# Kernel optimization log

Hardware: AMD Instinct MI355X
Metric: run time of the kernel (lower is better)

## Reference

```python
import jax, jax.numpy as jnp
import numpy as np

R, T, XD, ZD = 4096, 2048, 8, 8
G_INIT = 4.595


def setup_inputs() -> dict:
    key = jax.random.key(0)
    k1, k2, k3, k4, k5 = jax.random.split(key, 5)
    X_t = jax.random.normal(k1, (T, XD), dtype=jnp.float32)
    Z_t = jax.random.normal(k2, (T, ZD), dtype=jnp.float32)
    G = jnp.full((R,), G_INIT, dtype=jnp.float32)
    eta = jnp.abs(jax.random.normal(k3, (R, XD), dtype=jnp.float32))
    zeta = jax.random.normal(k4, (R, ZD), dtype=jnp.float32)
    gamma = jax.random.normal(k5, (R, ZD), dtype=jnp.float32)
    return {"X_t": X_t, "Z_t": Z_t, "G": G, "eta": eta, "zeta": zeta, "gamma": gamma}


def _forward(X_t, Z_t, G, eta, zeta, gamma):
    # addSigmoid=True (training path): G_hat = sigmoid(G)
    G_hat = jax.nn.sigmoid(G)                       # [R]
    x_term = jnp.einsum('tx,rx->rt', X_t, eta)      # [R,T]  X_t . eta per run
    z_term = jnp.einsum('tz,rz->rt', Z_t, zeta)     # [R,T]  Z_t . zeta per run
    b = jnp.einsum('tz,rz->rt', Z_t, gamma)         # [R,T]  Z_t . gamma per run
    # theta_t = G_hat * theta_{t-1} + b_{t-1}, theta_0 = 0
    c = jnp.concatenate([jnp.zeros((b.shape[0], 1), b.dtype), b[:, :-1]], axis=1)
    a = jnp.broadcast_to(G_hat[:, None], c.shape)
    def combine(e1, e2):
        a1, u1 = e1
        a2, u2 = e2
        return (a1 * a2, a2 * u1 + u2)
    _, theta = jax.lax.associative_scan(combine, (a, c), axis=1)  # [R,T]
    return theta + x_term + z_term


def reference(X_t, Z_t, G, eta, zeta, gamma):
    return _forward(X_t, Z_t, G, eta, zeta, gamma)
```

## Files before the change

### kernel.cpp

```cpp
#include <hip/hip_runtime.h>
#include <math.h>

typedef float  f32x4  __attribute__((ext_vector_type(4)));
typedef short  bf16x8 __attribute__((ext_vector_type(8)));

namespace {
constexpr int R_RUNS  = 4096;
constexpr int T_STEPS = 2048;
constexpr int NKS     = 3;
constexpr size_t PA_ELEMS = (size_t)(R_RUNS / 16) * NKS * 4 * 16 * 8;
}

__device__ __forceinline__ float sigmoidf_(float x) { return 1.0f / (1.0f + expf(-x)); }

__device__ __forceinline__ unsigned short f2bf(float f) {
    unsigned u = __float_as_uint(f);
    unsigned r = (u + 0x7FFFu + ((u >> 16) & 1u)) >> 16;
    return (unsigned short)r;
}
__device__ __forceinline__ float bf2f(unsigned short h) {
    return __uint_as_float(((unsigned)h) << 16);
}
__device__ __forceinline__ float powg(float gh, int e) {
    float w = 1.f, p = gh;
    #pragma unroll
    for (int i = 0; i < 6; ++i) { w *= ((e >> i) & 1) ? p : 1.f; p *= p; }
    return w;
}

extern "C" __global__ __launch_bounds__(256)
void dlm_k1_pack(const float* __restrict__ Xt, const float* __restrict__ Zt,
                 const float* __restrict__ G, const float* __restrict__ eta,
                 const float* __restrict__ zeta, const float* __restrict__ gamma,
                 unsigned short* __restrict__ Pa, unsigned short* __restrict__ Qb)
{
    const int tid  = threadIdx.x;
    const int wid  = tid >> 6;
    const int lane = tid & 63;

    if (blockIdx.x >= 8) {
        const int pw = (blockIdx.x - 8) * 4 + wid;
        const int r  = pw * 64 + lane;
        const float4 e0 = *reinterpret_cast<const float4*>(eta   + (size_t)r * 8);
        const float4 e1 = *reinterpret_cast<const float4*>(eta   + (size_t)r * 8 + 4);
        const float4 c0 = *reinterpret_cast<const float4*>(zeta  + (size_t)r * 8);
        const float4 c1 = *reinterpret_cast<const float4*>(zeta  + (size_t)r * 8 + 4);
        const float4 m0 = *reinterpret_cast<const float4*>(gamma + (size_t)r * 8);
        const float4 m1 = *reinterpret_cast<const float4*>(gamma + (size_t)r * 8 + 4);
        const float pr[24] = {e0.x, e0.y, e0.z, e0.w, e1.x, e1.y, e1.z, e1.w,
                              c0.x, c0.y, c0.z, c0.w, c1.x, c1.y, c1.z, c1.w,
                              m0.x, m0.y, m0.z, m0.w, m1.x, m1.y, m1.z, m1.w};
        const int rt = r >> 4, rw = r & 15;
        #pragma unroll
        for (int s = 0; s < NKS; ++s) {
            #pragma unroll
            for (int ko = 0; ko < 4; ++ko) {
                union { unsigned short u[8]; uint4 v; } pk;
                #pragma unroll
                for (int i = 0; i < 8; ++i) {
                    const int k = s * 32 + ko * 8 + i;
                    unsigned short o;
                    if (k < 24)      o = f2bf(pr[k]);
                    else if (k < 48) o = f2bf(pr[k - 24]);
                    else if (k < 72) { const unsigned short h = f2bf(pr[k - 48]);
                                       o = f2bf(pr[k - 48] - bf2f(h)); }
                    else             o = 0;
                    pk.u[i] = o;
                }
                *reinterpret_cast<uint4*>(Pa + ((size_t)((rt * NKS + s) * 4 + ko) * 16 + rw) * 8) = pk.v;
            }
        }
        return;
    }

    const int wv = blockIdx.x * 4 + wid;
    const int t  = wv * 64 + lane;

    const float gh = sigmoidf_(G[0]);
    float gh64 = gh;
    #pragma unroll
    for (int i = 0; i < 6; ++i) gh64 *= gh64;

    const float4 za = *reinterpret_cast<const float4*>(Zt + (size_t)t * 8);
    const float4 zb = *reinterpret_cast<const float4*>(Zt + (size_t)t * 8 + 4);
    const float4 xa = *reinterpret_cast<const float4*>(Xt + (size_t)t * 8);
    const float4 xb = *reinterpret_cast<const float4*>(Xt + (size_t)t * 8 + 4);

    float acc[8] = {0.f, 0.f, 0.f, 0.f, 0.f, 0.f, 0.f, 0.f};
    for (int m = 0; m < wv; ++m) {
        const float* __restrict__ zp = Zt + (size_t)(m * 64 + lane) * 8;
        const float4 pa = *reinterpret_cast<const float4*>(zp);
        const float4 pb = *reinterpret_cast<const float4*>(zp + 4);
        acc[0] = fmaf(gh64, acc[0], pa.x);
        acc[1] = fmaf(gh64, acc[1], pa.y);
        acc[2] = fmaf(gh64, acc[2], pa.z);
        acc[3] = fmaf(gh64, acc[3], pa.w);
        acc[4] = fmaf(gh64, acc[4], pb.x);
        acc[5] = fmaf(gh64, acc[5], pb.y);
        acc[6] = fmaf(gh64, acc[6], pb.z);
        acc[7] = fmaf(gh64, acc[7], pb.w);
    }
    const float wl = powg(gh, 63 - lane);
    #pragma unroll
    for (int i = 0; i < 8; ++i) acc[i] *= wl;
    #pragma unroll
    for (int d = 1; d < 64; d <<= 1) {
        #pragma unroll
        for (int i = 0; i < 8; ++i)
            acc[i] += __shfl_xor(acc[i], d, 64);
    }

    float I[8] = {za.x, za.y, za.z, za.w, zb.x, zb.y, zb.z, zb.w};
    float p = gh;
    #pragma unroll
    for (int d = 1; d < 64; d <<= 1) {
        #pragma unroll
        for (int i = 0; i < 8; ++i) {
            const float up = __shfl_up(I[i], (unsigned)d, 64);
            if (lane >= d) I[i] = fmaf(p, up, I[i]);
        }
        p *= p;
    }

    const float wj = powg(gh, lane);
    float Wt[8];
    #pragma unroll
    for (int i = 0; i < 8; ++i) {
        const float L = __shfl_up(I[i], 1u, 64);
        Wt[i] = fmaf(wj, acc[i], (lane == 0) ? 0.0f : L);
    }

    const float q[24] = {xa.x, xa.y, xa.z, xa.w, xb.x, xb.y, xb.z, xb.w,
                         za.x, za.y, za.z, za.w, zb.x, zb.y, zb.z, zb.w,
                         Wt[0], Wt[1], Wt[2], Wt[3], Wt[4], Wt[5], Wt[6], Wt[7]};
    const int tt = t >> 4, c = t & 15;
    #pragma unroll
    for (int s = 0; s < NKS; ++s) {
        #pragma unroll
        for (int ko = 0; ko < 4; ++ko) {
            union { unsigned short u[8]; uint4 v; } pk;
            #pragma unroll
            for (int i = 0; i < 8; ++i) {
                const int k = s * 32 + ko * 8 + i;
                unsigned short o;
                if (k < 24)      o = f2bf(q[k]);
                else if (k < 48) { const unsigned short h = f2bf(q[k - 24]);
                                   o = f2bf(q[k - 24] - bf2f(h)); }
                else if (k < 72) o = f2bf(q[k - 48]);
                else             o = 0;
                pk.u[i] = o;
            }
            *reinterpret_cast<uint4*>(Qb + ((size_t)((tt * NKS + s) * 4 + ko) * 16 + c) * 8) = pk.v;
        }
    }
}

extern "C" __global__ __launch_bounds__(256)
void dlm_kb_mfma(const float* __restrict__ Xt, const float* __restrict__ Zt,
                 const float* __restrict__ G, const float* __restrict__ eta,
                 const float* __restrict__ zeta, const float* __restrict__ gamma,
                 const unsigned short* __restrict__ Pa,
                 const unsigned short* __restrict__ Qb,
                 float* __restrict__ out)
{
    const int tid  = threadIdx.x;
    const int wid  = tid >> 6;
    const int lane = tid & 63;
    const int w    = blockIdx.x * 4 + wid;
    const int rt0  = (w & 127) * 2;
    const int tt0  = (w >> 7) * 2;
    const int r0   = rt0 * 16;
    const int t0   = tt0 * 16;

    const float G0 = G[0];
    const float gv = G[r0 + (lane & 31)];
    const bool uni = (__ballot(gv == G0) == ~0ull);

    if (uni) {
        const int ko = lane >> 4;
        const int rc = lane & 15;

        bf16x8 af[2][NKS], bfr[2][NKS];
        #pragma unroll
        for (int i = 0; i < 2; ++i)
            #pragma unroll
            for (int s = 0; s < NKS; ++s) {
                af[i][s] = *reinterpret_cast<const bf16x8*>(
                    Pa + ((size_t)(((rt0 + i) * NKS + s) * 4 + ko) * 16 + rc) * 8);
                bfr[i][s] = *reinterpret_cast<const bf16x8*>(
                    Qb + ((size_t)(((tt0 + i) * NKS + s) * 4 + ko) * 16 + rc) * 8);
            }

        f32x4 accv[2][2];
        #pragma unroll
        for (int i = 0; i < 2; ++i)
            #pragma unroll
            for (int j = 0; j < 2; ++j)
                accv[i][j] = (f32x4){0.f, 0.f, 0.f, 0.f};

        #pragma unroll
        for (int s = 0; s < NKS; ++s)
            #pragma unroll
            for (int i = 0; i < 2; ++i)
                #pragma unroll
                for (int j = 0; j < 2; ++j)
                    accv[i][j] = __builtin_amdgcn_mfma_f32_16x16x32_bf16(
                        af[i][s], bfr[j][s], accv[i][j], 0, 0, 0);

        const int orow = (lane >> 4) * 4;
        const int ocol = lane & 15;
        #pragma unroll
        for (int i = 0; i < 2; ++i)
            #pragma unroll
            for (int j = 0; j < 2; ++j)
                #pragma unroll
                for (int qv = 0; qv < 4; ++qv)
                    __builtin_nontemporal_store(
                        accv[i][j][qv],
                        &out[(size_t)(r0 + 16 * i + orow + qv) * T_STEPS + t0 + 16 * j + ocol]);
    } else {
        const int t = t0 + (lane & 31);
        const float4 fxa = *reinterpret_cast<const float4*>(Xt + (size_t)t * 8);
        const float4 fxb = *reinterpret_cast<const float4*>(Xt + (size_t)t * 8 + 4);
        const float4 fza = *reinterpret_cast<const float4*>(Zt + (size_t)t * 8);
        const float4 fzb = *reinterpret_cast<const float4*>(Zt + (size_t)t * 8 + 4);
        for (int rr = 0; rr < 32; ++rr) {
            const int r = r0 + rr;
            const float ghr = sigmoidf_(G[r]);
            const float* __restrict__ gc = gamma + (size_t)r * 8;
            const float* __restrict__ e  = eta   + (size_t)r * 8;
            const float* __restrict__ zc = zeta  + (size_t)r * 8;
            float th = 0.0f, mine = 0.0f;
            for (int s2 = 1; s2 <= t0 + 31; ++s2) {
                const float* __restrict__ zr = Zt + (size_t)(s2 - 1) * 8;
                float b = zr[0] * gc[0];
                #pragma unroll
                for (int qq = 1; qq < 8; ++qq) b = fmaf(zr[qq], gc[qq], b);
                th = fmaf(ghr, th, b);
                mine = (s2 == t) ? th : mine;
            }
            float s = mine;
            s = fmaf(fxa.x, e[0], s);  s = fmaf(fxa.y, e[1], s);
            s = fmaf(fxa.z, e[2], s);  s = fmaf(fxa.w, e[3], s);
            s = fmaf(fxb.x, e[4], s);  s = fmaf(fxb.y, e[5], s);
            s = fmaf(fxb.z, e[6], s);  s = fmaf(fxb.w, e[7], s);
            s = fmaf(fza.x, zc[0], s); s = fmaf(fza.y, zc[1], s);
            s = fmaf(fza.z, zc[2], s); s = fmaf(fza.w, zc[3], s);
            s = fmaf(fzb.x, zc[4], s); s = fmaf(fzb.y, zc[5], s);
            s = fmaf(fzb.z, zc[6], s); s = fmaf(fzb.w, zc[7], s);
            if (lane < 32) out[(size_t)r * T_STEPS + t] = s;
        }
    }
}

extern "C" void kernel_launch(void* const* d_in, const int* in_sizes, int n_in,
                              void* d_out, int out_size, void* d_ws, size_t ws_size,
                              hipStream_t stream)
{
    const float* Xt    = (const float*)d_in[0];
    const float* Zt    = (const float*)d_in[1];
    const float* G     = (const float*)d_in[2];
    const float* eta   = (const float*)d_in[3];
    const float* zeta  = (const float*)d_in[4];
    const float* gamma = (const float*)d_in[5];
    float* out = (float*)d_out;

    unsigned short* Pa = (unsigned short*)d_ws;
    unsigned short* Qb = Pa + PA_ELEMS;

    const dim3 blk(256);
    dlm_k1_pack<<<dim3(24),   blk, 0, stream>>>(Xt, Zt, G, eta, zeta, gamma, Pa, Qb);
    dlm_kb_mfma<<<dim3(2048), blk, 0, stream>>>(Xt, Zt, G, eta, zeta, gamma, Pa, Qb, out);
}
```

Baseline: 20.40 us.

## Give each wave a 16-run by 256-step strip with transposed float4 stores

Each wavefront now owns one 16-row run tile and loops over 16 time tiles. It keeps the run-side MFMA operand in registers and loads only the time-side operand per tile. The MFMA operands are swapped so each lane holds 4 consecutive time steps, which allows a single 16-byte nontemporal store instead of four scalar stores. The grid shrinks from 2048 to 512 blocks, trading parallelism for operand reuse, fewer store instructions and more per-wave serial work. The fallback scalar path is reworked to match the new tiling.

```diff
diff --git a/kernel.cpp b/kernel.cpp
--- a/kernel.cpp
+++ b/kernel.cpp
@@ -167,88 +167,78 @@
     const int wid  = tid >> 6;
     const int lane = tid & 63;
     const int w    = blockIdx.x * 4 + wid;
-    const int rt0  = (w & 127) * 2;
-    const int tt0  = (w >> 7) * 2;
-    const int r0   = rt0 * 16;
-    const int t0   = tt0 * 16;
+    const int rt   = w >> 3;
+    const int tc   = w & 7;
+    const int r0   = rt * 16;
+    const int tbase = tc * 256;
 
     const float G0 = G[0];
-    const float gv = G[r0 + (lane & 31)];
+    const float gv = G[r0 + (lane & 15)];
     const bool uni = (__ballot(gv == G0) == ~0ull);
 
     if (uni) {
         const int ko = lane >> 4;
         const int rc = lane & 15;
 
-        bf16x8 af[2][NKS], bfr[2][NKS];
-        #pragma unroll
-        for (int i = 0; i < 2; ++i)
-            #pragma unroll
-            for (int s = 0; s < NKS; ++s) {
-                af[i][s] = *reinterpret_cast<const bf16x8*>(
-                    Pa + ((size_t)(((rt0 + i) * NKS + s) * 4 + ko) * 16 + rc) * 8);
-                bfr[i][s] = *reinterpret_cast<const bf16x8*>(
-                    Qb + ((size_t)(((tt0 + i) * NKS + s) * 4 + ko) * 16 + rc) * 8);
-            }
-
-        f32x4 accv[2][2];
-        #pragma unroll
-        for (int i = 0; i < 2; ++i)
-            #pragma unroll
-            for (int j = 0; j < 2; ++j)
-                accv[i][j] = (f32x4){0.f, 0.f, 0.f, 0.f};
-
+        bf16x8 pf[NKS];
         #pragma unroll
         for (int s = 0; s < NKS; ++s)
-            #pragma unroll
-            for (int i = 0; i < 2; ++i)
-                #pragma unroll
-                for (int j = 0; j < 2; ++j)
-                    accv[i][j] = __builtin_amdgcn_mfma_f32_16x16x32_bf16(
-                        af[i][s], bfr[j][s], accv[i][j], 0, 0, 0);
+            pf[s] = *reinterpret_cast<const bf16x8*>(
+                Pa + ((size_t)((rt * NKS + s) * 4 + ko) * 16 + rc) * 8);
 
         const int orow = (lane >> 4) * 4;
         const int ocol = lane & 15;
-        #pragma unroll
-        for (int i = 0; i < 2; ++i)
-            #pragma unroll
-            for (int j = 0; j < 2; ++j)
-                #pragma unroll
-                for (int qv = 0; qv < 4; ++qv)
-                    __builtin_nontemporal_store(
-                        accv[i][j][qv],
-                        &out[(size_t)(r0 + 16 * i + orow + qv) * T_STEPS + t0 + 16 * j + ocol]);
+        float* __restrict__ obase = out + (size_t)(r0 + ocol) * T_STEPS + tbase + orow;
+
+        #pragma unroll 2
+        for (int it = 0; it < 16; ++it) {
+            const int tt = tc * 16 + it;
+            bf16x8 qf[NKS];
+            #pragma unroll
+            for (int s = 0; s < NKS; ++s)
+                qf[s] = *reinterpret_cast<const bf16x8*>(
+                    Qb + ((size_t)((tt * NKS + s) * 4 + ko) * 16 + rc) * 8);
+
+            f32x4 acc = (f32x4){0.f, 0.f, 0.f, 0.f};
+            #pragma unroll
+            for (int s = 0; s < NKS; ++s)
+                acc = __builtin_amdgcn_mfma_f32_16x16x32_bf16(qf[s], pf[s], acc, 0, 0, 0);
+
+            __builtin_nontemporal_store(acc, reinterpret_cast<f32x4*>(obase + it * 16));
+        }
     } else {
-        const int t = t0 + (lane & 31);
-        const float4 fxa = *reinterpret_cast<const float4*>(Xt + (size_t)t * 8);
-        const float4 fxb = *reinterpret_cast<const float4*>(Xt + (size_t)t * 8 + 4);
-        const float4 fza = *reinterpret_cast<const float4*>(Zt + (size_t)t * 8);
-        const float4 fzb = *reinterpret_cast<const float4*>(Zt + (size_t)t * 8 + 4);
-        for (int rr = 0; rr < 32; ++rr) {
+        for (int rr = 0; rr < 16; ++rr) {
             const int r = r0 + rr;
             const float ghr = sigmoidf_(G[r]);
             const float* __restrict__ gc = gamma + (size_t)r * 8;
             const float* __restrict__ e  = eta   + (size_t)r * 8;
             const float* __restrict__ zc = zeta  + (size_t)r * 8;
-            float th = 0.0f, mine = 0.0f;
-            for (int s2 = 1; s2 <= t0 + 31; ++s2) {
+            float th = 0.0f;
+            float mine[4] = {0.f, 0.f, 0.f, 0.f};
+            const int tend = tbase + 256;
+            for (int s2 = 1; s2 <= tend; ++s2) {
                 const float* __restrict__ zr = Zt + (size_t)(s2 - 1) * 8;
                 float b = zr[0] * gc[0];
                 #pragma unroll
                 for (int qq = 1; qq < 8; ++qq) b = fmaf(zr[qq], gc[qq], b);
                 th = fmaf(ghr, th, b);
-                mine = (s2 == t) ? th : mine;
-            }
-            float s = mine;
-            s = fmaf(fxa.x, e[0], s);  s = fmaf(fxa.y, e[1], s);
-            s = fmaf(fxa.z, e[2], s);  s = fmaf(fxa.w, e[3], s);
-            s = fmaf(fxb.x, e[4], s);  s = fmaf(fxb.y, e[5], s);
-            s = fmaf(fxb.z, e[6], s);  s = fmaf(fxb.w, e[7], s);
-            s = fmaf(fza.x, zc[0], s); s = fmaf(fza.y, zc[1], s);
-            s = fmaf(fza.z, zc[2], s); s = fmaf(fza.w, zc[3], s);
-            s = fmaf(fzb.x, zc[4], s); s = fmaf(fzb.y, zc[5], s);
-            s = fmaf(fzb.z, zc[6], s); s = fmaf(fzb.w, zc[7], s);
-            if (lane < 32) out[(size_t)r * T_STEPS + t] = s;
+                #pragma unroll
+                for (int qv = 0; qv < 4; ++qv)
+                    if (s2 == tbase + qv * 64 + lane) mine[qv] = th;
+            }
+            #pragma unroll
+            for (int qv = 0; qv < 4; ++qv) {
+                const int t = tbase + qv * 64 + lane;
+                const float* __restrict__ xr = Xt + (size_t)t * 8;
+                const float* __restrict__ zr = Zt + (size_t)t * 8;
+                float s = mine[qv];
+                #pragma unroll
+                for (int qq = 0; qq < 8; ++qq) {
+                    s = fmaf(xr[qq], e[qq], s);
+                    s = fmaf(zr[qq], zc[qq], s);
+                }
+                out[(size_t)r * T_STEPS + t] = s;
+            }
         }
     }
 }
@@ -269,6 +259,6 @@
     unsigned short* Qb = Pa + PA_ELEMS;
 
     const dim3 blk(256);
-    dlm_k1_pack<<<dim3(24),   blk, 0, stream>>>(Xt, Zt, G, eta, zeta, gamma, Pa, Qb);
-    dlm_kb_mfma<<<dim3(2048), blk, 0, stream>>>(Xt, Zt, G, eta, zeta, gamma, Pa, Qb, out);
-}
+    dlm_k1_pack<<<dim3(24),  blk, 0, stream>>>(Xt, Zt, G, eta, zeta, gamma, Pa, Qb);
+    dlm_kb_mfma<<<dim3(512), blk, 0, stream>>>(Xt, Zt, G, eta, zeta, gamma, Pa, Qb, out);
+}
```

Result: slower. 25.01 us (+22.6%).
